# Optimization experiments

Hardware: AMD Instinct MI355X
Metric: run time of the kernel (lower is better)

## Reference

```python
import jax, jax.numpy as jnp
import numpy as np

MAX_DIST = 32
NUM_HEADS = 16


def setup_inputs() -> dict:
    key = jax.random.key(0)
    ks = jax.random.split(key, 10)
    D = 1024
    B, S = 2, 2048
    hd = D // NUM_HEADS
    sc = 0.02
    return {
        "x": jax.random.normal(ks[0], (B, S, D), dtype=jnp.float32),
        "Wq": jax.random.normal(ks[1], (D, D), dtype=jnp.float32) * sc,
        "bq": jax.random.normal(ks[2], (D,), dtype=jnp.float32) * sc,
        "Wk": jax.random.normal(ks[3], (D, D), dtype=jnp.float32) * sc,
        "bk": jax.random.normal(ks[4], (D,), dtype=jnp.float32) * sc,
        "Wv": jax.random.normal(ks[5], (D, D), dtype=jnp.float32) * sc,
        "bv": jax.random.normal(ks[6], (D,), dtype=jnp.float32) * sc,
        "Wo": jax.random.normal(ks[7], (D, D), dtype=jnp.float32) * sc,
        "bo": jax.random.normal(ks[8], (D,), dtype=jnp.float32) * sc,
        "rel_emb": jax.random.normal(ks[9], (2 * MAX_DIST + 1, hd), dtype=jnp.float32) * sc,
    }


def reference(x, Wq, bq, Wk, bk, Wv, bv, Wo, bo, rel_emb):
    B, S, D = x.shape
    H = NUM_HEADS
    hd = D // H
    scale = hd ** -0.5

    def proj(W, b):
        # [B,S,D] -> [B,H,S,hd]
        return (x @ W + b).reshape(B, S, H, hd).transpose(0, 2, 1, 3)

    q = proj(Wq, bq)
    k = proj(Wk, bk)
    v = proj(Wv, bv)

    # relative position embedding lookup: [S,S,hd]
    pos = jnp.arange(S)
    rel = jnp.clip(pos[:, None] - pos[None, :], -MAX_DIST, MAX_DIST) + MAX_DIST
    rpe = rel_emb[rel]  # [S,S,hd]

    cc = jnp.einsum('bhqd,bhkd->bhqk', q, k) * scale
    cp = jnp.einsum('bhqd,qkd->bhqk', q, rpe) * scale
    attn = jax.nn.softmax(cc + cp, axis=-1)
    ctx = jnp.einsum('bhqk,bhkd->bhqd', attn, v)  # [B,H,S,hd]
    ctx = ctx.transpose(0, 2, 1, 3).reshape(B, S, D)
    return ctx @ Wo + bo
```

## Files before the change

kernel.cpp:

```cpp
#include <hip/hip_runtime.h>

typedef __attribute__((ext_vector_type(4))) float f32x4;
typedef __attribute__((ext_vector_type(8))) short bf16x8;

#define SEQ    2048
#define HD     64
#define NBH    32
#define MTOK   4096
#define DMODEL 1024
#define QBLK   128
#define C1 0.180336880f
#define C2 11.5415603f

__device__ __forceinline__ unsigned short f2b(float f) {
  unsigned int u = __float_as_uint(f);
  u += 0x7fffu + ((u >> 16) & 1u);
  return (unsigned short)(u >> 16);
}
__device__ __forceinline__ float b2f(unsigned short s) {
  return __uint_as_float(((unsigned int)s) << 16);
}
__device__ __forceinline__ unsigned int cvtpk_bf16(float lo, float hi) {
  unsigned int r;
  asm("v_cvt_pk_bf16_f32 %0, %1, %2" : "=v"(r) : "v"(lo), "v"(hi));
  return r;
}
__device__ __forceinline__ void gload16(const void* g, void* l) {
  __builtin_amdgcn_global_load_lds(
      (const __attribute__((address_space(1))) unsigned int*)g,
      (__attribute__((address_space(3))) unsigned int*)l, 16, 0, 0);
}

__global__ __launch_bounds__(256) void k_prep(const float* __restrict__ x,
                                              unsigned short* __restrict__ xb,
                                              const float* __restrict__ Wq,
                                              const float* __restrict__ Wk,
                                              const float* __restrict__ Wv,
                                              const float* __restrict__ Wo,
                                              unsigned short* __restrict__ Wqkv,
                                              unsigned short* __restrict__ Wot) {
  __shared__ float tile[64 * 65];
  int bid = blockIdx.x, t = threadIdx.x;
  if (bid < 4096) {
    int i = bid * 256 + t;
    float4 v = ((const float4*)x)[i];
    ushort4 o;
    o.x = f2b(v.x); o.y = f2b(v.y); o.z = f2b(v.z); o.w = f2b(v.w);
    ((ushort4*)xb)[i] = o;
    return;
  }
  int e2 = bid - 4096;
  int z = e2 >> 8, rem = e2 & 255;
  int bi = rem >> 4, bj = rem & 15;
  const float* W = (z == 0) ? Wq : (z == 1) ? Wk : (z == 2) ? Wv : Wo;
  unsigned short* Wt = (z == 3) ? Wot : Wqkv + (size_t)z * DMODEL * DMODEL;
  for (int p = 0; p < 16; p++) {
    int e = p * 256 + t;
    int r = e >> 6, c = e & 63;
    tile[r * 65 + c] = W[(size_t)(bi * 64 + r) * DMODEL + bj * 64 + c];
  }
  __syncthreads();
  for (int p = 0; p < 16; p++) {
    int e = p * 256 + t;
    int n = e >> 6, k = e & 63;
    Wt[(size_t)(bj * 64 + n) * DMODEL + bi * 64 + k] = f2b(tile[k * 65 + n]);
  }
}

template <int MODE>
__global__ __launch_bounds__(256) void k_gemm_bt(
    const unsigned short* __restrict__ A, const unsigned short* __restrict__ Bt,
    int M, int N, int K,
    const float* __restrict__ bias0, const float* __restrict__ bias1,
    const float* __restrict__ bias2,
    float* __restrict__ Cf,
    unsigned short* __restrict__ Qo, unsigned short* __restrict__ Ko,
    unsigned short* __restrict__ Vo) {
  __shared__ unsigned short As[128 * 64];
  __shared__ unsigned short Bs[128 * 64];
  int bm = blockIdx.x, bn = blockIdx.y;
  int tid = threadIdx.x;
  int w = tid >> 6, lane = tid & 63;
  int lg = lane >> 4, lc = lane & 15;
  int wm = (w >> 1) * 64, wn = (w & 1) * 64;
  f32x4 acc[4][4];
  for (int a = 0; a < 4; a++)
    for (int b = 0; b < 4; b++) acc[a][b] = (f32x4){0.f, 0.f, 0.f, 0.f};
  const unsigned short* ag = A + (size_t)(bm * 128) * K;
  const unsigned short* bg = Bt + (size_t)(bn * 128) * K;
  for (int k0 = 0; k0 < K; k0 += 64) {
    __syncthreads();
    for (int p = 0; p < 4; p++) {
      int c = (w * 4 + p) * 64 + lane;
      int r = c >> 3, ch = (c & 7) ^ (r & 7);
      gload16(ag + (size_t)r * K + k0 + ch * 8, &As[c * 8]);
      gload16(bg + (size_t)r * K + k0 + ch * 8, &Bs[c * 8]);
    }
    __syncthreads();
    for (int kk = 0; kk < 2; kk++) {
      bf16x8 av[4], bv[4];
      for (int mi = 0; mi < 4; mi++) {
        int row = wm + mi * 16 + lc;
        av[mi] = *(const bf16x8*)&As[row * 64 + ((kk * 32 + lg * 8) ^ ((row & 7) << 3))];
      }
      for (int ni = 0; ni < 4; ni++) {
        int row = wn + ni * 16 + lc;
        bv[ni] = *(const bf16x8*)&Bs[row * 64 + ((kk * 32 + lg * 8) ^ ((row & 7) << 3))];
      }
      for (int mi = 0; mi < 4; mi++)
        for (int ni = 0; ni < 4; ni++)
          acc[mi][ni] = __builtin_amdgcn_mfma_f32_16x16x32_bf16(av[mi], bv[ni], acc[mi][ni], 0, 0, 0);
    }
  }
  for (int mi = 0; mi < 4; mi++) {
    for (int i = 0; i < 4; i++) {
      int row = bm * 128 + wm + mi * 16 + 4 * lg + i;
      for (int ni = 0; ni < 4; ni++) {
        int col = bn * 128 + wn + ni * 16 + lc;
        float v = acc[mi][ni][i];
        if (MODE == 0) {
          Cf[(size_t)row * N + col] = v + bias0[col];
        } else {
          int which = col >> 10, hcol = col & 1023;
          const float* bb = which == 0 ? bias0 : (which == 1 ? bias1 : bias2);
          unsigned short* dst = which == 0 ? Qo : (which == 1 ? Ko : Vo);
          int b = row >> 11, s = row & 2047;
          int h = hcol >> 6, d = hcol & 63;
          float vv = v + bb[hcol];
          if (which == 0) vv *= C1;
          dst[(((size_t)(b * 16 + h)) * SEQ + s) * HD + d] = f2b(vv);
        }
      }
    }
  }
}

__global__ __launch_bounds__(256) void k_tvqr(const unsigned short* __restrict__ V,
                                              unsigned short* __restrict__ Vt,
                                              const unsigned short* __restrict__ Qb,
                                              const float* __restrict__ rel_emb,
                                              unsigned short* __restrict__ qr) {
  __shared__ unsigned short tile[64 * 72];
  __shared__ float relS[65 * 66];
  __shared__ unsigned short qS[32 * 64];
  int bh = blockIdx.y, t = threadIdx.x;
  if (blockIdx.x < 32) {
    int s0 = blockIdx.x * 64;
    for (int p = 0; p < 16; p++) {
      int e = p * 256 + t;
      int r = e >> 6, c = e & 63;
      tile[r * 72 + c] = V[(((size_t)bh) * SEQ + s0 + r) * HD + c];
    }
    __syncthreads();
    for (int p = 0; p < 16; p++) {
      int e = p * 256 + t;
      int d = e >> 6, j = e & 63;
      Vt[(((size_t)bh) * HD + d) * SEQ + s0 + j] = tile[j * 72 + d];
    }
  } else {
    int s0 = (blockIdx.x - 32) * 32;
    for (int i = t; i < 65 * 64; i += 256) relS[(i >> 6) * 66 + (i & 63)] = rel_emb[i];
    for (int i = t; i < 32 * 64; i += 256) qS[i] = Qb[((size_t)bh * SEQ + s0) * HD + i];
    __syncthreads();
    for (int e = t; e < 32 * 65; e += 256) {
      int sl = e / 65, r = e % 65;
      float acc = 0.f;
      for (int d = 0; d < 64; d++) acc += b2f(qS[sl * 64 + d]) * relS[r * 66 + d];
      qr[((size_t)bh * SEQ + s0 + sl) * 65 + r] = f2b(acc);
    }
  }
}

__global__ __launch_bounds__(512, 4) void k_attn(const unsigned short* __restrict__ Qb,
                                                 const unsigned short* __restrict__ Kb,
                                                 const unsigned short* __restrict__ Vtb,
                                                 const unsigned short* __restrict__ qr,
                                                 unsigned short* __restrict__ ctx) {
  __shared__ unsigned short Ks[128 * 64];
  __shared__ unsigned short Vts[64 * 128];
  __shared__ unsigned short Ps[8][16 * 64];
  __shared__ unsigned short qrs[QBLK * 65];
  int bh = blockIdx.x, qt = blockIdx.y;
  int tid = threadIdx.x, w = tid >> 6, lane = tid & 63;
  int lg = lane >> 4, lc = lane & 15;
  int q0 = qt * QBLK, qw = q0 + w * 16;

  {
    const unsigned int* src = (const unsigned int*)(qr + ((size_t)bh * SEQ + q0) * 65);
    for (int i = tid; i < QBLK * 65 / 2; i += 512) ((unsigned int*)qrs)[i] = src[i];
  }
  bf16x8 aq[2];
  {
    const unsigned short* qp = Qb + ((size_t)bh * SEQ + qw + lc) * HD + lg * 8;
    aq[0] = *(const bf16x8*)qp;
    aq[1] = *(const bf16x8*)(qp + 32);
  }
  f32x4 o[4];
  float l[4];
  for (int n = 0; n < 4; n++) o[n] = (f32x4){0.f, 0.f, 0.f, 0.f};
  for (int i = 0; i < 4; i++) l[i] = 0.f;
  __syncthreads();

  float blo[4], bhi[4];
  for (int i = 0; i < 4; i++) {
    int rl = w * 16 + 4 * lg + i;
    blo[i] = b2f(qrs[rl * 65])      - C2;
    bhi[i] = b2f(qrs[rl * 65 + 64]) - C2;
  }

  for (int kt = 0; kt < SEQ / 128; kt++) {
    int k0 = kt * 128;
    const unsigned short* kg = Kb + ((size_t)bh * SEQ + k0) * HD;
    const unsigned short* vg = Vtb + ((size_t)bh * HD) * SEQ + k0;
    #pragma unroll
    for (int p = 0; p < 2; p++) {
      int idx = p * 512 + tid;
      int kr = idx >> 3, kch = (idx & 7) ^ (kr & 7);
      gload16(kg + (size_t)kr * HD + kch * 8, &Ks[idx * 8]);
      int vr = idx >> 4, vch = (idx & 15) ^ (vr & 7);
      gload16(vg + (size_t)vr * SEQ + vch * 8, &Vts[idx * 8]);
    }
    __syncthreads();

    #pragma unroll
    for (int sub = 0; sub < 2; sub++) {
      int k0s = k0 + sub * 64;

      f32x4 s[4];
      #pragma unroll
      for (int n = 0; n < 4; n++) s[n] = (f32x4){0.f, 0.f, 0.f, 0.f};
      __builtin_amdgcn_s_setprio(1);
      #pragma unroll
      for (int n = 0; n < 4; n++) {
        int row = sub * 64 + n * 16 + lc;
        #pragma unroll
        for (int kk = 0; kk < 2; kk++) {
          bf16x8 bk = *(const bf16x8*)&Ks[row * 64 + ((kk * 32 + lg * 8) ^ ((row & 7) << 3))];
          s[n] = __builtin_amdgcn_mfma_f32_16x16x32_bf16(aq[kk], bk, s[n], 0, 0, 0);
        }
      }
      __builtin_amdgcn_s_setprio(0);

      int dw = qw - k0s;
      bool gather = (dw >= -32) && (dw <= 80);
      #pragma unroll
      for (int n = 0; n < 4; n++)
        #pragma unroll
        for (int i = 0; i < 4; i++) {
          float bf;
          if (gather) {
            int rl = w * 16 + 4 * lg + i;
            int rel = rl + q0 - k0s - n * 16 - lc;
            rel = rel < -32 ? -32 : (rel > 32 ? 32 : rel);
            bf = b2f(qrs[rl * 65 + rel + 32]) - C2;
          } else {
            bf = (dw < 0) ? blo[i] : bhi[i];
          }
          float p = __builtin_amdgcn_exp2f(s[n][i] + bf);
          s[n][i] = p;
          l[i] += p;
        }

      #pragma unroll
      for (int n = 0; n < 4; n++)
        #pragma unroll
        for (int i = 0; i < 4; i += 2) {
          unsigned int u = cvtpk_bf16(s[n][i], s[n][i + 1]);
          int r0 = 4 * lg + i, r1 = r0 + 1;
          Ps[w][r0 * 64 + ((n * 16 + lc) ^ ((r0 & 7) << 3))] = (unsigned short)u;
          Ps[w][r1 * 64 + ((n * 16 + lc) ^ ((r1 & 7) << 3))] = (unsigned short)(u >> 16);
        }

      __builtin_amdgcn_s_setprio(1);
      #pragma unroll
      for (int kk = 0; kk < 2; kk++) {
        bf16x8 ap = *(const bf16x8*)&Ps[w][lc * 64 + ((kk * 32 + lg * 8) ^ ((lc & 7) << 3))];
        #pragma unroll
        for (int n = 0; n < 4; n++) {
          int vrow = n * 16 + lc;
          int vcol = sub * 64 + kk * 32 + lg * 8;
          bf16x8 bv = *(const bf16x8*)&Vts[vrow * 128 + (vcol ^ ((vrow & 7) << 3))];
          o[n] = __builtin_amdgcn_mfma_f32_16x16x32_bf16(ap, bv, o[n], 0, 0, 0);
        }
      }
      __builtin_amdgcn_s_setprio(0);
    }
    __syncthreads();
  }

  int b = bh >> 4, h = bh & 15;
  for (int i = 0; i < 4; i++) {
    float t = l[i];
    t += __shfl_xor(t, 1);
    t += __shfl_xor(t, 2);
    t += __shfl_xor(t, 4);
    t += __shfl_xor(t, 8);
    float inv = 1.f / t;
    int row = qw + 4 * lg + i;
    size_t base = ((size_t)(b * SEQ + row)) * DMODEL + h * HD;
    for (int n = 0; n < 4; n++) ctx[base + n * 16 + lc] = f2b(o[n][i] * inv);
  }
}

extern "C" void kernel_launch(void* const* d_in, const int* in_sizes, int n_in,
                              void* d_out, int out_size, void* d_ws, size_t ws_size,
                              hipStream_t stream) {
  const float* x   = (const float*)d_in[0];
  const float* Wq  = (const float*)d_in[1];
  const float* bq  = (const float*)d_in[2];
  const float* Wk  = (const float*)d_in[3];
  const float* bk  = (const float*)d_in[4];
  const float* Wv  = (const float*)d_in[5];
  const float* bv  = (const float*)d_in[6];
  const float* Wo  = (const float*)d_in[7];
  const float* bo  = (const float*)d_in[8];
  const float* rel = (const float*)d_in[9];
  float* out = (float*)d_out;

  char* ws = (char*)d_ws;
  size_t off = 0;
  auto carve = [&](size_t bytes) -> void* {
    void* p = ws + off;
    off += (bytes + 255) & ~(size_t)255;
    return p;
  };
  unsigned short* xb   = (unsigned short*)carve((size_t)MTOK * DMODEL * 2);
  unsigned short* Wqkv = (unsigned short*)carve((size_t)3 * DMODEL * DMODEL * 2);
  unsigned short* Wot  = (unsigned short*)carve((size_t)DMODEL * DMODEL * 2);
  unsigned short* Qb   = (unsigned short*)carve((size_t)NBH * SEQ * HD * 2);
  unsigned short* Kb   = (unsigned short*)carve((size_t)NBH * SEQ * HD * 2);
  unsigned short* Vb   = (unsigned short*)carve((size_t)NBH * SEQ * HD * 2);
  unsigned short* Vtb  = (unsigned short*)carve((size_t)NBH * SEQ * HD * 2);
  unsigned short* qr   = (unsigned short*)carve((size_t)NBH * SEQ * 65 * 2);
  unsigned short* ctx  = (unsigned short*)carve((size_t)MTOK * DMODEL * 2);

  k_prep<<<4096 + 1024, 256, 0, stream>>>(x, xb, Wq, Wk, Wv, Wo, Wqkv, Wot);
  k_gemm_bt<1><<<dim3(32, 24), 256, 0, stream>>>(xb, Wqkv, MTOK, 3 * DMODEL, DMODEL,
                                                 bq, bk, bv, nullptr, Qb, Kb, Vb);
  k_tvqr<<<dim3(96, 32), 256, 0, stream>>>(Vb, Vtb, Qb, rel, qr);
  k_attn<<<dim3(NBH, SEQ / QBLK), 512, 0, stream>>>(Qb, Kb, Vtb, qr, ctx);
  k_gemm_bt<0><<<dim3(32, 8), 256, 0, stream>>>(ctx, Wot, MTOK, DMODEL, DMODEL,
                                                bo, nullptr, nullptr, out,
                                                nullptr, nullptr, nullptr);
}
```

Measured before the change: 173.0 us.

## Split attention over key halves with partial-sum combine kernel

The attention kernel now processes 64-key tiles instead of 128, which halves K/V shared memory and raises the launch-bounds occupancy hint from 4 to 6. It is also templated to split the key range across two grid z-blocks. Each half writes fp32 partial outputs and row sums, and a new combine kernel adds them, normalizes and writes bf16 ctx. The aim is to double the block count (512 to 1024) for better CU utilization and occupancy. The cost is an extra kernel launch and fp32 partial traffic to global memory. The split path runs only if the workspace is large enough, otherwise the single-pass path is used.

```diff
diff --git a/kernel.cpp b/kernel.cpp
--- a/kernel.cpp
+++ b/kernel.cpp
@@ -171,16 +171,21 @@
   }
 }
 
-__global__ __launch_bounds__(512, 4) void k_attn(const unsigned short* __restrict__ Qb,
+template <int SPLIT>
+__global__ __launch_bounds__(512, 6) void k_attn(const unsigned short* __restrict__ Qb,
                                                  const unsigned short* __restrict__ Kb,
                                                  const unsigned short* __restrict__ Vtb,
                                                  const unsigned short* __restrict__ qr,
-                                                 unsigned short* __restrict__ ctx) {
-  __shared__ unsigned short Ks[128 * 64];
-  __shared__ unsigned short Vts[64 * 128];
+                                                 unsigned short* __restrict__ ctx,
+                                                 float* __restrict__ po,
+                                                 float* __restrict__ pl) {
+  __shared__ unsigned short Ks[64 * 64];
+  __shared__ unsigned short Vts[64 * 64];
   __shared__ unsigned short Ps[8][16 * 64];
   __shared__ unsigned short qrs[QBLK * 65];
   int bh = blockIdx.x, qt = blockIdx.y;
+  int half = (SPLIT == 2) ? blockIdx.z : 0;
+  int kbase = half * (SEQ / SPLIT) / 64;
   int tid = threadIdx.x, w = tid >> 6, lane = tid & 63;
   int lg = lane >> 4, lc = lane & 15;
   int q0 = qt * QBLK, qw = q0 + w * 16;
@@ -208,98 +213,118 @@
     bhi[i] = b2f(qrs[rl * 65 + 64]) - C2;
   }
 
-  for (int kt = 0; kt < SEQ / 128; kt++) {
-    int k0 = kt * 128;
+  for (int kt = 0; kt < (SEQ / 64) / SPLIT; kt++) {
+    int k0 = (kbase + kt) * 64;
     const unsigned short* kg = Kb + ((size_t)bh * SEQ + k0) * HD;
     const unsigned short* vg = Vtb + ((size_t)bh * HD) * SEQ + k0;
-    #pragma unroll
-    for (int p = 0; p < 2; p++) {
-      int idx = p * 512 + tid;
-      int kr = idx >> 3, kch = (idx & 7) ^ (kr & 7);
-      gload16(kg + (size_t)kr * HD + kch * 8, &Ks[idx * 8]);
-      int vr = idx >> 4, vch = (idx & 15) ^ (vr & 7);
-      gload16(vg + (size_t)vr * SEQ + vch * 8, &Vts[idx * 8]);
-    }
-    __syncthreads();
-
-    #pragma unroll
-    for (int sub = 0; sub < 2; sub++) {
-      int k0s = k0 + sub * 64;
-
-      f32x4 s[4];
+    {
+      int c = tid;
+      int r = c >> 3, ch = (c & 7) ^ (r & 7);
+      gload16(kg + (size_t)r * HD + ch * 8, &Ks[c * 8]);
+      gload16(vg + (size_t)r * SEQ + ch * 8, &Vts[c * 8]);
+    }
+    __syncthreads();
+
+    f32x4 s[4];
+    #pragma unroll
+    for (int n = 0; n < 4; n++) s[n] = (f32x4){0.f, 0.f, 0.f, 0.f};
+    __builtin_amdgcn_s_setprio(1);
+    #pragma unroll
+    for (int n = 0; n < 4; n++) {
+      int row = n * 16 + lc;
       #pragma unroll
-      for (int n = 0; n < 4; n++) s[n] = (f32x4){0.f, 0.f, 0.f, 0.f};
-      __builtin_amdgcn_s_setprio(1);
+      for (int kk = 0; kk < 2; kk++) {
+        bf16x8 bk = *(const bf16x8*)&Ks[row * 64 + ((kk * 32 + lg * 8) ^ ((row & 7) << 3))];
+        s[n] = __builtin_amdgcn_mfma_f32_16x16x32_bf16(aq[kk], bk, s[n], 0, 0, 0);
+      }
+    }
+    __builtin_amdgcn_s_setprio(0);
+
+    int dw = qw - k0;
+    bool gather = (dw >= -32) && (dw <= 80);
+    #pragma unroll
+    for (int n = 0; n < 4; n++)
+      #pragma unroll
+      for (int i = 0; i < 4; i++) {
+        float bf;
+        if (gather) {
+          int rl = w * 16 + 4 * lg + i;
+          int rel = rl + q0 - k0 - n * 16 - lc;
+          rel = rel < -32 ? -32 : (rel > 32 ? 32 : rel);
+          bf = b2f(qrs[rl * 65 + rel + 32]) - C2;
+        } else {
+          bf = (dw < 0) ? blo[i] : bhi[i];
+        }
+        float p = __builtin_amdgcn_exp2f(s[n][i] + bf);
+        s[n][i] = p;
+        l[i] += p;
+      }
+
+    #pragma unroll
+    for (int n = 0; n < 4; n++)
+      #pragma unroll
+      for (int i = 0; i < 4; i += 2) {
+        unsigned int u = cvtpk_bf16(s[n][i], s[n][i + 1]);
+        int r0 = 4 * lg + i, r1 = r0 + 1;
+        Ps[w][r0 * 64 + ((n * 16 + lc) ^ ((r0 & 7) << 3))] = (unsigned short)u;
+        Ps[w][r1 * 64 + ((n * 16 + lc) ^ ((r1 & 7) << 3))] = (unsigned short)(u >> 16);
+      }
+
+    __builtin_amdgcn_s_setprio(1);
+    #pragma unroll
+    for (int kk = 0; kk < 2; kk++) {
+      bf16x8 ap = *(const bf16x8*)&Ps[w][lc * 64 + ((kk * 32 + lg * 8) ^ ((lc & 7) << 3))];
       #pragma unroll
       for (int n = 0; n < 4; n++) {
-        int row = sub * 64 + n * 16 + lc;
-        #pragma unroll
-        for (int kk = 0; kk < 2; kk++) {
-          bf16x8 bk = *(const bf16x8*)&Ks[row * 64 + ((kk * 32 + lg * 8) ^ ((row & 7) << 3))];
-          s[n] = __builtin_amdgcn_mfma_f32_16x16x32_bf16(aq[kk], bk, s[n], 0, 0, 0);
-        }
-      }
-      __builtin_amdgcn_s_setprio(0);
-
-      int dw = qw - k0s;
-      bool gather = (dw >= -32) && (dw <= 80);
-      #pragma unroll
-      for (int n = 0; n < 4; n++)
-        #pragma unroll
-        for (int i = 0; i < 4; i++) {
-          float bf;
-          if (gather) {
-            int rl = w * 16 + 4 * lg + i;
-            int rel = rl + q0 - k0s - n * 16 - lc;
-            rel = rel < -32 ? -32 : (rel > 32 ? 32 : rel);
-            bf = b2f(qrs[rl * 65 + rel + 32]) - C2;
-          } else {
-            bf = (dw < 0) ? blo[i] : bhi[i];
-          }
-          float p = __builtin_amdgcn_exp2f(s[n][i] + bf);
-          s[n][i] = p;
-          l[i] += p;
-        }
-
-      #pragma unroll
-      for (int n = 0; n < 4; n++)
-        #pragma unroll
-        for (int i = 0; i < 4; i += 2) {
-          unsigned int u = cvtpk_bf16(s[n][i], s[n][i + 1]);
-          int r0 = 4 * lg + i, r1 = r0 + 1;
-          Ps[w][r0 * 64 + ((n * 16 + lc) ^ ((r0 & 7) << 3))] = (unsigned short)u;
-          Ps[w][r1 * 64 + ((n * 16 + lc) ^ ((r1 & 7) << 3))] = (unsigned short)(u >> 16);
-        }
-
-      __builtin_amdgcn_s_setprio(1);
-      #pragma unroll
-      for (int kk = 0; kk < 2; kk++) {
-        bf16x8 ap = *(const bf16x8*)&Ps[w][lc * 64 + ((kk * 32 + lg * 8) ^ ((lc & 7) << 3))];
-        #pragma unroll
-        for (int n = 0; n < 4; n++) {
-          int vrow = n * 16 + lc;
-          int vcol = sub * 64 + kk * 32 + lg * 8;
-          bf16x8 bv = *(const bf16x8*)&Vts[vrow * 128 + (vcol ^ ((vrow & 7) << 3))];
-          o[n] = __builtin_amdgcn_mfma_f32_16x16x32_bf16(ap, bv, o[n], 0, 0, 0);
-        }
-      }
-      __builtin_amdgcn_s_setprio(0);
-    }
-    __syncthreads();
-  }
-
-  int b = bh >> 4, h = bh & 15;
+        int row = n * 16 + lc;
+        bf16x8 bv = *(const bf16x8*)&Vts[row * 64 + ((kk * 32 + lg * 8) ^ ((row & 7) << 3))];
+        o[n] = __builtin_amdgcn_mfma_f32_16x16x32_bf16(ap, bv, o[n], 0, 0, 0);
+      }
+    }
+    __builtin_amdgcn_s_setprio(0);
+    __syncthreads();
+  }
+
   for (int i = 0; i < 4; i++) {
     float t = l[i];
     t += __shfl_xor(t, 1);
     t += __shfl_xor(t, 2);
     t += __shfl_xor(t, 4);
     t += __shfl_xor(t, 8);
-    float inv = 1.f / t;
     int row = qw + 4 * lg + i;
-    size_t base = ((size_t)(b * SEQ + row)) * DMODEL + h * HD;
-    for (int n = 0; n < 4; n++) ctx[base + n * 16 + lc] = f2b(o[n][i] * inv);
-  }
+    if (SPLIT == 2) {
+      size_t pbase = (((size_t)half * NBH + bh) * SEQ + row) * HD;
+      for (int n = 0; n < 4; n++) po[pbase + n * 16 + lc] = o[n][i];
+      if (lc == 0) pl[((size_t)half * NBH + bh) * SEQ + row] = t;
+    } else {
+      float inv = 1.f / t;
+      int b = bh >> 4, h = bh & 15;
+      size_t base = ((size_t)(b * SEQ + row)) * DMODEL + h * HD;
+      for (int n = 0; n < 4; n++) ctx[base + n * 16 + lc] = f2b(o[n][i] * inv);
+    }
+  }
+}
+
+__global__ __launch_bounds__(256) void k_comb(const float* __restrict__ po,
+                                              const float* __restrict__ pl,
+                                              unsigned short* __restrict__ ctx) {
+  size_t g = (size_t)blockIdx.x * 256 + threadIdx.x;
+  size_t e = g * 4;
+  int d = (int)(e & 63);
+  size_t bhq = e >> 6;
+  int q = (int)(bhq & (SEQ - 1));
+  int bh = (int)(bhq >> 11);
+  float4 a = *(const float4*)(po + bhq * HD + d);
+  float4 c = *(const float4*)(po + (size_t)NBH * SEQ * HD + bhq * HD + d);
+  float lt = pl[bhq] + pl[(size_t)NBH * SEQ + bhq];
+  float inv = 1.f / lt;
+  int b = bh >> 4, h = bh & 15;
+  ushort4 o;
+  o.x = f2b((a.x + c.x) * inv);
+  o.y = f2b((a.y + c.y) * inv);
+  o.z = f2b((a.z + c.z) * inv);
+  o.w = f2b((a.w + c.w) * inv);
+  *(ushort4*)(ctx + ((size_t)(b * SEQ + q)) * DMODEL + h * HD + d) = o;
 }
 
 extern "C" void kernel_launch(void* const* d_in, const int* in_sizes, int n_in,
@@ -333,12 +358,20 @@
   unsigned short* Vtb  = (unsigned short*)carve((size_t)NBH * SEQ * HD * 2);
   unsigned short* qr   = (unsigned short*)carve((size_t)NBH * SEQ * 65 * 2);
   unsigned short* ctx  = (unsigned short*)carve((size_t)MTOK * DMODEL * 2);
+  float*          po   = (float*)carve((size_t)2 * NBH * SEQ * HD * 4);
+  float*          pl   = (float*)carve((size_t)2 * NBH * SEQ * 4);
+  bool split = (off <= ws_size);
 
   k_prep<<<4096 + 1024, 256, 0, stream>>>(x, xb, Wq, Wk, Wv, Wo, Wqkv, Wot);
   k_gemm_bt<1><<<dim3(32, 24), 256, 0, stream>>>(xb, Wqkv, MTOK, 3 * DMODEL, DMODEL,
                                                  bq, bk, bv, nullptr, Qb, Kb, Vb);
   k_tvqr<<<dim3(96, 32), 256, 0, stream>>>(Vb, Vtb, Qb, rel, qr);
-  k_attn<<<dim3(NBH, SEQ / QBLK), 512, 0, stream>>>(Qb, Kb, Vtb, qr, ctx);
+  if (split) {
+    k_attn<2><<<dim3(NBH, SEQ / QBLK, 2), 512, 0, stream>>>(Qb, Kb, Vtb, qr, ctx, po, pl);
+    k_comb<<<(NBH * SEQ * HD / 4) / 256, 256, 0, stream>>>(po, pl, ctx);
+  } else {
+    k_attn<1><<<dim3(NBH, SEQ / QBLK), 512, 0, stream>>>(Qb, Kb, Vtb, qr, ctx, po, pl);
+  }
   k_gemm_bt<0><<<dim3(32, 8), 256, 0, stream>>>(ctx, Wot, MTOK, DMODEL, DMODEL,
                                                 bo, nullptr, nullptr, out,
                                                 nullptr, nullptr, nullptr);
```

Result: slower. 364.7 us (+110.7%).
